# Kernel optimization log

Hardware: AMD Instinct MI355X
Metric: run time of the kernel (lower is better)

Reference implementation:

```python
import jax, jax.numpy as jnp
import numpy as np

N, E = 50000, 800000
D_IN, D_H, D_E, D_P = 128, 64, 64, 64


def _glorot(key, shape):
    lim = (6.0 / (shape[0] + shape[1])) ** 0.5
    return jax.random.uniform(key, shape, jnp.float32, -lim, lim)


def setup_inputs() -> dict:
    key = jax.random.key(0)
    ks = jax.random.split(key, 8)
    x = jax.random.normal(ks[0], (N, D_IN), jnp.float32)
    edge_index = jax.random.randint(ks[1], (2, E), 0, N, dtype=jnp.int64)
    return {
        "x": x,
        "edge_index": edge_index,
        "W1": _glorot(ks[2], (D_IN, D_H)),
        "b1": jnp.zeros((D_H,), jnp.float32),
        "W2": _glorot(ks[3], (D_H, D_E)),
        "b2": jnp.zeros((D_E,), jnp.float32),
        "Wp1": _glorot(ks[4], (D_E, D_E)),
        "bp1": jnp.zeros((D_E,), jnp.float32),
        "Wp2": _glorot(ks[5], (D_E, D_P)),
        "bp2": jnp.zeros((D_P,), jnp.float32),
    }


def gcn_conv(x, src, dst, W, b):
    # PyG GCNConv: h = D^{-1/2}(A+I)D^{-1/2} (x W) + b, self-loops already in src/dst
    n = x.shape[0]
    h = x @ W  # transform first (out_dim < in_dim -> cheaper messages)
    deg = jax.ops.segment_sum(jnp.ones_like(dst, dtype=h.dtype), dst, num_segments=n)
    dinv = jnp.where(deg > 0, jax.lax.rsqrt(deg), 0.0)
    norm = dinv[src] * dinv[dst]  # [E']
    out = jax.ops.segment_sum(h[src] * norm[:, None], dst, num_segments=n)
    return out + b


def reference(x, edge_index, W1, b1, W2, b2, Wp1, bp1, Wp2, bp2):
    n = x.shape[0]
    loops = jnp.arange(n, dtype=edge_index.dtype)
    src = jnp.concatenate([edge_index[0], loops])
    dst = jnp.concatenate([edge_index[1], loops])
    h = jax.nn.relu(gcn_conv(x, src, dst, W1, b1))
    z = gcn_conv(h, src, dst, W2, b2)
    p = jax.nn.relu(z @ Wp1 + bp1) @ Wp2 + bp2
    return (z, p)
```

## Files before the change

### kernel.cpp

```cpp
#include <hip/hip_runtime.h>
#include <hip/hip_fp16.h>

#define DIN 128
#define DH 64
#define NBINS 512
#define BIN_SHIFT 7
#define BIN_NODES 128
#define ETILE 4096
#define EBUF 4096

__device__ inline unsigned pack_half2(float a, float b) {
  __half2 h = __floats2half2_rn(a, b);
  return *(unsigned*)&h;
}
__device__ inline float2 unpack_half2(unsigned u) {
  __half2 h = *(__half2*)&u;
  return __half22float2(h);
}

__global__ __launch_bounds__(512) void k_zero(int* __restrict__ p, int n) {
  int i = blockIdx.x * blockDim.x + threadIdx.x;
  if (i < n) p[i] = 0;
}

__global__ __launch_bounds__(256) void k_fusedA(const float* __restrict__ x,
                                                const float* __restrict__ W1,
                                                __half* __restrict__ g1,
                                                const int* __restrict__ dst,
                                                int* __restrict__ binTot,
                                                int n, int e, int gG) {
  __shared__ float xsT[32][132];
  __shared__ float ws[32 * 64];
  __shared__ int hh[NBINS];
  int t = threadIdx.x;
  int bid = blockIdx.x;

  if (bid >= gG) {
    int b = bid - gG;
    for (int i = t; i < NBINS; i += 256) hh[i] = 0;
    __syncthreads();
    int lo = b * ETILE, hi = lo + ETILE; if (hi > e) hi = e;
    for (int i = lo + t; i < hi; i += 256) atomicAdd(&hh[dst[i] >> BIN_SHIFT], 1);
    __syncthreads();
    for (int i = t; i < NBINS; i += 256) if (hh[i]) atomicAdd(&binTot[i], hh[i]);
    return;
  }

  int row0 = bid * 128;
  int rg = t >> 4, cg = t & 15;
  int r0 = rg * 8, c0 = cg * 4;
  int lr = t >> 3, kq = t & 7;
  float4 acc[8];
#pragma unroll
  for (int i = 0; i < 8; ++i) acc[i] = make_float4(0.f, 0.f, 0.f, 0.f);

  for (int kc = 0; kc < DIN; kc += 32) {
#pragma unroll
    for (int it = 0; it < 4; ++it) {
      int r = it * 32 + lr;
      int gr = row0 + r;
      float4 v = make_float4(0.f, 0.f, 0.f, 0.f);
      if (gr < n) v = *(const float4*)&x[(size_t)gr * DIN + kc + kq * 4];
      xsT[kq * 4 + 0][r] = v.x;
      xsT[kq * 4 + 1][r] = v.y;
      xsT[kq * 4 + 2][r] = v.z;
      xsT[kq * 4 + 3][r] = v.w;
    }
#pragma unroll
    for (int j = 0; j < 8; ++j) ws[t + j * 256] = W1[(size_t)kc * 64 + t + j * 256];
    __syncthreads();
#pragma unroll
    for (int k = 0; k < 32; ++k) {
      float4 xa = *(const float4*)&xsT[k][r0];
      float4 xb = *(const float4*)&xsT[k][r0 + 4];
      float4 wv = *(const float4*)&ws[k * 64 + c0];
      float xr[8] = {xa.x, xa.y, xa.z, xa.w, xb.x, xb.y, xb.z, xb.w};
#pragma unroll
      for (int i = 0; i < 8; ++i) {
        acc[i].x = fmaf(xr[i], wv.x, acc[i].x);
        acc[i].y = fmaf(xr[i], wv.y, acc[i].y);
        acc[i].z = fmaf(xr[i], wv.z, acc[i].z);
        acc[i].w = fmaf(xr[i], wv.w, acc[i].w);
      }
    }
    __syncthreads();
  }
#pragma unroll
  for (int i = 0; i < 8; ++i) {
    int gr = row0 + r0 + i;
    if (gr < n) {
      uint2 u;
      u.x = pack_half2(acc[i].x, acc[i].y);
      u.y = pack_half2(acc[i].z, acc[i].w);
      *(uint2*)&g1[(size_t)gr * 64 + c0] = u;
    }
  }
}

__global__ __launch_bounds__(512) void k_binscan(const int* __restrict__ binTot,
                                                 int* __restrict__ binOff,
                                                 int* __restrict__ binCur, int e) {
  __shared__ int sm[NBINS];
  int t = threadIdx.x;
  int v = binTot[t];
  sm[t] = v;
  __syncthreads();
  for (int ofs = 1; ofs < NBINS; ofs <<= 1) {
    int u = (t >= ofs) ? sm[t - ofs] : 0;
    __syncthreads();
    sm[t] += u;
    __syncthreads();
  }
  int ex = sm[t] - v;
  binOff[t] = ex;
  binCur[t] = ex;
  if (t == NBINS - 1) binOff[NBINS] = sm[NBINS - 1];
}

__global__ __launch_bounds__(256) void k_scatter2(const int* __restrict__ src,
                                                  const int* __restrict__ dst,
                                                  int* __restrict__ binCur,
                                                  int* __restrict__ sp, int e) {
  __shared__ int hh[NBINS];
  __shared__ int base[NBINS];
  int t = threadIdx.x;
  for (int i = t; i < NBINS; i += 256) hh[i] = 0;
  __syncthreads();
  int lo = blockIdx.x * ETILE, hi = lo + ETILE; if (hi > e) hi = e;
  for (int i = lo + t; i < hi; i += 256) atomicAdd(&hh[dst[i] >> BIN_SHIFT], 1);
  __syncthreads();
  for (int i = t; i < NBINS; i += 256) {
    int c = hh[i];
    base[i] = c ? atomicAdd(&binCur[i], c) : 0;
  }
  __syncthreads();
  for (int i = t; i < NBINS; i += 256) hh[i] = 0;
  __syncthreads();
  for (int i = lo + t; i < hi; i += 256) {
    int d = dst[i];
    int bn = d >> BIN_SHIFT;
    int pos = base[bn] + atomicAdd(&hh[bn], 1);
    sp[pos] = (src[i] << BIN_SHIFT) | (d & (BIN_NODES - 1));
  }
}

__global__ __launch_bounds__(256) void k_bincsr(const int* __restrict__ sp,
                                                const int* __restrict__ binOff,
                                                int* __restrict__ off,
                                                float* __restrict__ dinv,
                                                int* __restrict__ srcs,
                                                int n, int e) {
  __shared__ int dl[BIN_NODES];
  __shared__ int sc[BIN_NODES];
  __shared__ int curl[BIN_NODES];
  __shared__ int ebuf[EBUF];
  int b = blockIdx.x, t = threadIdx.x;
  if (t < BIN_NODES) dl[t] = 0;
  __syncthreads();
  int e0 = binOff[b];
  int e1 = binOff[b + 1];
  for (int i = e0 + t; i < e1; i += 256) {
    int u = sp[i];
    int k = i - e0;
    if (k < EBUF) ebuf[k] = u;
    atomicAdd(&dl[u & (BIN_NODES - 1)], 1);
  }
  __syncthreads();
  if (t < BIN_NODES) sc[t] = dl[t];
  __syncthreads();
  for (int ofs = 1; ofs < BIN_NODES; ofs <<= 1) {
    int v = (t < BIN_NODES && t >= ofs) ? sc[t - ofs] : 0;
    __syncthreads();
    if (t < BIN_NODES) sc[t] += v;
    __syncthreads();
  }
  int nbase = b * BIN_NODES;
  if (t < BIN_NODES) {
    int ex = e0 + sc[t] - dl[t];
    curl[t] = ex;
    int node = nbase + t;
    if (node < n) {
      off[node] = ex;
      dinv[node] = rsqrtf((float)(dl[t] + 1));
    }
  }
  if (b == 0 && t == 0) off[n] = e;
  __syncthreads();
  for (int i = e0 + t; i < e1; i += 256) {
    int k = i - e0;
    int u = (k < EBUF) ? ebuf[k] : sp[i];
    int l = u & (BIN_NODES - 1);
    int pos = atomicAdd(&curl[l], 1);
    srcs[pos] = u >> BIN_SHIFT;
  }
}

__global__ __launch_bounds__(256) void k_agg(const __half* __restrict__ gh,
                                             const int* __restrict__ off,
                                             const int* __restrict__ srcs,
                                             const float* __restrict__ dinv,
                                             const float* __restrict__ bias,
                                             __half* __restrict__ out, int n, int relu) {
  int gid = blockIdx.x * 4 + (threadIdx.x >> 6);
  if (gid >= n) return;
  gid = __builtin_amdgcn_readfirstlane(gid);
  int lane = threadIdx.x & 63;
  int grp = lane >> 4;
  int d4 = (lane & 15) * 4;
  float di = dinv[gid];
  float4 acc = make_float4(0.f, 0.f, 0.f, 0.f);
  if (grp == 0) {
    uint2 raw = *(const uint2*)(gh + (size_t)gid * DH + d4);
    float2 f0 = unpack_half2(raw.x), f1 = unpack_half2(raw.y);
    float s = di * di;
    acc.x = f0.x * s; acc.y = f0.y * s; acc.z = f1.x * s; acc.w = f1.y * s;
  }
  int b0 = off[gid], b1 = off[gid + 1];
  int j = b0 + grp;
  for (; j + 12 < b1; j += 16) {
    int s0 = srcs[j], s1 = srcs[j + 4], s2 = srcs[j + 8], s3 = srcs[j + 12];
    float w0 = dinv[s0] * di, w1 = dinv[s1] * di;
    float w2 = dinv[s2] * di, w3 = dinv[s3] * di;
    uint2 r0 = *(const uint2*)(gh + (size_t)s0 * DH + d4);
    uint2 r1 = *(const uint2*)(gh + (size_t)s1 * DH + d4);
    uint2 r2 = *(const uint2*)(gh + (size_t)s2 * DH + d4);
    uint2 r3 = *(const uint2*)(gh + (size_t)s3 * DH + d4);
    float2 a0 = unpack_half2(r0.x), a1 = unpack_half2(r0.y);
    float2 c0 = unpack_half2(r1.x), c1 = unpack_half2(r1.y);
    float2 e0 = unpack_half2(r2.x), e1 = unpack_half2(r2.y);
    float2 g0 = unpack_half2(r3.x), g1 = unpack_half2(r3.y);
    acc.x = fmaf(a0.x, w0, acc.x); acc.y = fmaf(a0.y, w0, acc.y);
    acc.z = fmaf(a1.x, w0, acc.z); acc.w = fmaf(a1.y, w0, acc.w);
    acc.x = fmaf(c0.x, w1, acc.x); acc.y = fmaf(c0.y, w1, acc.y);
    acc.z = fmaf(c1.x, w1, acc.z); acc.w = fmaf(c1.y, w1, acc.w);
    acc.x = fmaf(e0.x, w2, acc.x); acc.y = fmaf(e0.y, w2, acc.y);
    acc.z = fmaf(e1.x, w2, acc.z); acc.w = fmaf(e1.y, w2, acc.w);
    acc.x = fmaf(g0.x, w3, acc.x); acc.y = fmaf(g0.y, w3, acc.y);
    acc.z = fmaf(g1.x, w3, acc.z); acc.w = fmaf(g1.y, w3, acc.w);
  }
  for (; j + 4 < b1; j += 8) {
    int sa = srcs[j], sb = srcs[j + 4];
    float wa = dinv[sa] * di, wb = dinv[sb] * di;
    uint2 ra = *(const uint2*)(gh + (size_t)sa * DH + d4);
    uint2 rb = *(const uint2*)(gh + (size_t)sb * DH + d4);
    float2 a0 = unpack_half2(ra.x), a1 = unpack_half2(ra.y);
    float2 c0 = unpack_half2(rb.x), c1 = unpack_half2(rb.y);
    acc.x = fmaf(a0.x, wa, acc.x); acc.y = fmaf(a0.y, wa, acc.y);
    acc.z = fmaf(a1.x, wa, acc.z); acc.w = fmaf(a1.y, wa, acc.w);
    acc.x = fmaf(c0.x, wb, acc.x); acc.y = fmaf(c0.y, wb, acc.y);
    acc.z = fmaf(c1.x, wb, acc.z); acc.w = fmaf(c1.y, wb, acc.w);
  }
  if (j < b1) {
    int s = srcs[j];
    float w = dinv[s] * di;
    uint2 r = *(const uint2*)(gh + (size_t)s * DH + d4);
    float2 f0 = unpack_half2(r.x), f1 = unpack_half2(r.y);
    acc.x = fmaf(f0.x, w, acc.x); acc.y = fmaf(f0.y, w, acc.y);
    acc.z = fmaf(f1.x, w, acc.z); acc.w = fmaf(f1.y, w, acc.w);
  }
  acc.x += __shfl_xor(acc.x, 16, 64); acc.x += __shfl_xor(acc.x, 32, 64);
  acc.y += __shfl_xor(acc.y, 16, 64); acc.y += __shfl_xor(acc.y, 32, 64);
  acc.z += __shfl_xor(acc.z, 16, 64); acc.z += __shfl_xor(acc.z, 32, 64);
  acc.w += __shfl_xor(acc.w, 16, 64); acc.w += __shfl_xor(acc.w, 32, 64);
  if (lane < 16) {
    if (bias) {
      float4 bv = *(const float4*)&bias[d4];
      acc.x += bv.x; acc.y += bv.y; acc.z += bv.z; acc.w += bv.w;
    }
    if (relu) {
      acc.x = fmaxf(acc.x, 0.f); acc.y = fmaxf(acc.y, 0.f);
      acc.z = fmaxf(acc.z, 0.f); acc.w = fmaxf(acc.w, 0.f);
    }
    uint2 u;
    u.x = pack_half2(acc.x, acc.y);
    u.y = pack_half2(acc.z, acc.w);
    *(uint2*)&out[(size_t)gid * DH + d4] = u;
  }
}

__global__ __launch_bounds__(256) void k_head3(const __half* __restrict__ ah,
                                               const float* __restrict__ W2,
                                               const float* __restrict__ b2,
                                               const float* __restrict__ Wp1,
                                               const float* __restrict__ bp1,
                                               const float* __restrict__ Wp2,
                                               const float* __restrict__ bp2,
                                               float* __restrict__ z,
                                               float* __restrict__ p, int n) {
  constexpr int KC = 32;
  constexpr int MP = 132;
  __shared__ float xsT[KC][MP];
  __shared__ float ws[KC * 64];
  __shared__ float TsT[64][MP];
  int t = threadIdx.x;
  int row0 = blockIdx.x * 128;
  int rg = t >> 4, cg = t & 15;
  int r0 = rg * 8, c0 = cg * 4;
  int lr = t >> 3, kq = t & 7;

  float4 acc[8];
#pragma unroll
  for (int i = 0; i < 8; ++i) acc[i] = make_float4(0.f, 0.f, 0.f, 0.f);
  for (int kc = 0; kc < 64; kc += KC) {
#pragma unroll
    for (int it = 0; it < 4; ++it) {
      int r = it * 32 + lr;
      int gr = row0 + r;
      uint2 v = make_uint2(0u, 0u);
      if (gr < n) v = *(const uint2*)(ah + (size_t)gr * 64 + kc + kq * 4);
      float2 f0 = unpack_half2(v.x), f1 = unpack_half2(v.y);
      xsT[kq * 4 + 0][r] = f0.x;
      xsT[kq * 4 + 1][r] = f0.y;
      xsT[kq * 4 + 2][r] = f1.x;
      xsT[kq * 4 + 3][r] = f1.y;
    }
#pragma unroll
    for (int j = 0; j < 8; ++j) ws[t + j * 256] = W2[(size_t)kc * 64 + t + j * 256];
    __syncthreads();
#pragma unroll
    for (int k = 0; k < KC; ++k) {
      float4 xa = *(const float4*)&xsT[k][r0];
      float4 xb = *(const float4*)&xsT[k][r0 + 4];
      float4 wv = *(const float4*)&ws[k * 64 + c0];
      float xr[8] = {xa.x, xa.y, xa.z, xa.w, xb.x, xb.y, xb.z, xb.w};
#pragma unroll
      for (int i = 0; i < 8; ++i) {
        acc[i].x = fmaf(xr[i], wv.x, acc[i].x);
        acc[i].y = fmaf(xr[i], wv.y, acc[i].y);
        acc[i].z = fmaf(xr[i], wv.z, acc[i].z);
        acc[i].w = fmaf(xr[i], wv.w, acc[i].w);
      }
    }
    __syncthreads();
  }
  {
    float4 bv = *(const float4*)&b2[c0];
#pragma unroll
    for (int i = 0; i < 8; ++i) {
      float4 o = acc[i];
      o.x += bv.x; o.y += bv.y; o.z += bv.z; o.w += bv.w;
      int r = r0 + i;
      int gr = row0 + r;
      if (gr < n) *(float4*)&z[(size_t)gr * 64 + c0] = o;
      TsT[c0 + 0][r] = o.x;
      TsT[c0 + 1][r] = o.y;
      TsT[c0 + 2][r] = o.z;
      TsT[c0 + 3][r] = o.w;
    }
  }

  float4 acc2[8];
#pragma unroll
  for (int i = 0; i < 8; ++i) acc2[i] = make_float4(0.f, 0.f, 0.f, 0.f);
  for (int kc = 0; kc < 64; kc += KC) {
    __syncthreads();
#pragma unroll
    for (int j = 0; j < 8; ++j) ws[t + j * 256] = Wp1[(size_t)kc * 64 + t + j * 256];
    __syncthreads();
#pragma unroll
    for (int k = 0; k < KC; ++k) {
      float4 xa = *(const float4*)&TsT[kc + k][r0];
      float4 xb = *(const float4*)&TsT[kc + k][r0 + 4];
      float4 wv = *(const float4*)&ws[k * 64 + c0];
      float xr[8] = {xa.x, xa.y, xa.z, xa.w, xb.x, xb.y, xb.z, xb.w};
#pragma unroll
      for (int i = 0; i < 8; ++i) {
        acc2[i].x = fmaf(xr[i], wv.x, acc2[i].x);
        acc2[i].y = fmaf(xr[i], wv.y, acc2[i].y);
        acc2[i].z = fmaf(xr[i], wv.z, acc2[i].z);
        acc2[i].w = fmaf(xr[i], wv.w, acc2[i].w);
      }
    }
  }
  __syncthreads();
  {
    float4 bv = *(const float4*)&bp1[c0];
#pragma unroll
    for (int i = 0; i < 8; ++i) {
      int r = r0 + i;
      TsT[c0 + 0][r] = fmaxf(acc2[i].x + bv.x, 0.f);
      TsT[c0 + 1][r] = fmaxf(acc2[i].y + bv.y, 0.f);
      TsT[c0 + 2][r] = fmaxf(acc2[i].z + bv.z, 0.f);
      TsT[c0 + 3][r] = fmaxf(acc2[i].w + bv.w, 0.f);
    }
  }

  float4 acc3[8];
#pragma unroll
  for (int i = 0; i < 8; ++i) acc3[i] = make_float4(0.f, 0.f, 0.f, 0.f);
  for (int kc = 0; kc < 64; kc += KC) {
    __syncthreads();
#pragma unroll
    for (int j = 0; j < 8; ++j) ws[t + j * 256] = Wp2[(size_t)kc * 64 + t + j * 256];
    __syncthreads();
#pragma unroll
    for (int k = 0; k < KC; ++k) {
      float4 xa = *(const float4*)&TsT[kc + k][r0];
      float4 xb = *(const float4*)&TsT[kc + k][r0 + 4];
      float4 wv = *(const float4*)&ws[k * 64 + c0];
      float xr[8] = {xa.x, xa.y, xa.z, xa.w, xb.x, xb.y, xb.z, xb.w};
#pragma unroll
      for (int i = 0; i < 8; ++i) {
        acc3[i].x = fmaf(xr[i], wv.x, acc3[i].x);
        acc3[i].y = fmaf(xr[i], wv.y, acc3[i].y);
        acc3[i].z = fmaf(xr[i], wv.z, acc3[i].z);
        acc3[i].w = fmaf(xr[i], wv.w, acc3[i].w);
      }
    }
  }
  {
    float4 bv = *(const float4*)&bp2[c0];
#pragma unroll
    for (int i = 0; i < 8; ++i) {
      int gr = row0 + r0 + i;
      if (gr < n) {
        float4 o = acc3[i];
        o.x += bv.x; o.y += bv.y; o.z += bv.z; o.w += bv.w;
        *(float4*)&p[(size_t)gr * 64 + c0] = o;
      }
    }
  }
}

extern "C" void kernel_launch(void* const* d_in, const int* in_sizes, int n_in,
                              void* d_out, int out_size, void* d_ws, size_t ws_size,
                              hipStream_t stream) {
  const float* x   = (const float*)d_in[0];
  const int*   ei  = (const int*)d_in[1];
  const float* W1  = (const float*)d_in[2];
  const float* b1  = (const float*)d_in[3];
  const float* W2  = (const float*)d_in[4];
  const float* b2  = (const float*)d_in[5];
  const float* Wp1 = (const float*)d_in[6];
  const float* bp1 = (const float*)d_in[7];
  const float* Wp2 = (const float*)d_in[8];
  const float* bp2 = (const float*)d_in[9];

  int n = in_sizes[0] / DIN;
  int e = in_sizes[1] / 2;
  const int* src = ei;
  const int* dst = ei + e;

  int nblkE = (e + ETILE - 1) / ETILE;
  int nbBins = (n + BIN_NODES - 1) / BIN_NODES;
  int gG = (n + 127) / 128;

  char* ws = (char*)d_ws;
  __half* gtab   = (__half*)ws;
  __half* htab   = (__half*)(ws + ((size_t)7 << 20));
  char*   ctrl   = ws + ((size_t)14 << 20);
  int*    binTot = (int*)(ctrl);
  int*    binOff = (int*)(ctrl + 4096);
  int*    binCur = (int*)(ctrl + 8192);
  int*    off    = (int*)(ctrl + 16384);
  float*  dinv   = (float*)(ctrl + 16384 + (1 << 18));
  int*    sp     = (int*)(ctrl + 16384 + (2 << 18));
  int*    srcs   = sp + e;

  float* zout = (float*)d_out;
  float* pout = zout + (size_t)n * DH;

  k_zero<<<1, 512, 0, stream>>>(binTot, NBINS);

  k_fusedA<<<gG + nblkE, 256, 0, stream>>>(x, W1, gtab, dst, binTot, n, e, gG);

  k_binscan<<<1, 512, 0, stream>>>(binTot, binOff, binCur, e);

  k_scatter2<<<nblkE, 256, 0, stream>>>(src, dst, binCur, sp, e);

  k_bincsr<<<nbBins, 256, 0, stream>>>(sp, binOff, off, dinv, srcs, n, e);

  k_agg<<<(n + 3) / 4, 256, 0, stream>>>(gtab, off, srcs, dinv, b1, htab, n, 1);

  k_agg<<<(n + 3) / 4, 256, 0, stream>>>(htab, off, srcs, dinv, nullptr, gtab, n, 0);

  k_head3<<<gG, 256, 0, stream>>>(gtab, W2, b2, Wp1, bp1, Wp2, bp2, zout, pout, n);
}
```

Baseline: 145.1 us.

## Replace tiled head MLP with per-row wavefront kernel reading weights from global

The three-layer head kernel, which used 128-row tiles with LDS-staged weights and block barriers, is replaced by a 64-thread kernel where each pair of lanes owns one row and half the output columns. Weights are read straight from global memory with float4 loads instead of being staged in shared memory, and no __syncthreads are needed because each wave handles its own rows. This removes barrier and staging overhead and gives many more small blocks. The cost is that every lane reloads the full weight rows through cache, a 32-float accumulator raises register pressure, and the z/p stores are strided per lane and less coalesced.

```diff
diff --git a/kernel.cpp b/kernel.cpp
--- a/kernel.cpp
+++ b/kernel.cpp
@@ -8,6 +8,7 @@
 #define BIN_NODES 128
 #define ETILE 4096
 #define EBUF 4096
+#define HROWS 32
 
 __device__ inline unsigned pack_half2(float a, float b) {
   __half2 h = __floats2half2_rn(a, b);
@@ -278,146 +279,115 @@
   }
 }
 
-__global__ __launch_bounds__(256) void k_head3(const __half* __restrict__ ah,
-                                               const float* __restrict__ W2,
-                                               const float* __restrict__ b2,
-                                               const float* __restrict__ Wp1,
-                                               const float* __restrict__ bp1,
-                                               const float* __restrict__ Wp2,
-                                               const float* __restrict__ bp2,
-                                               float* __restrict__ z,
-                                               float* __restrict__ p, int n) {
-  constexpr int KC = 32;
-  constexpr int MP = 132;
-  __shared__ float xsT[KC][MP];
-  __shared__ float ws[KC * 64];
-  __shared__ float TsT[64][MP];
-  int t = threadIdx.x;
-  int row0 = blockIdx.x * 128;
-  int rg = t >> 4, cg = t & 15;
-  int r0 = rg * 8, c0 = cg * 4;
-  int lr = t >> 3, kq = t & 7;
-
-  float4 acc[8];
-#pragma unroll
-  for (int i = 0; i < 8; ++i) acc[i] = make_float4(0.f, 0.f, 0.f, 0.f);
-  for (int kc = 0; kc < 64; kc += KC) {
-#pragma unroll
-    for (int it = 0; it < 4; ++it) {
-      int r = it * 32 + lr;
-      int gr = row0 + r;
-      uint2 v = make_uint2(0u, 0u);
-      if (gr < n) v = *(const uint2*)(ah + (size_t)gr * 64 + kc + kq * 4);
-      float2 f0 = unpack_half2(v.x), f1 = unpack_half2(v.y);
-      xsT[kq * 4 + 0][r] = f0.x;
-      xsT[kq * 4 + 1][r] = f0.y;
-      xsT[kq * 4 + 2][r] = f1.x;
-      xsT[kq * 4 + 3][r] = f1.y;
-    }
-#pragma unroll
-    for (int j = 0; j < 8; ++j) ws[t + j * 256] = W2[(size_t)kc * 64 + t + j * 256];
-    __syncthreads();
-#pragma unroll
-    for (int k = 0; k < KC; ++k) {
-      float4 xa = *(const float4*)&xsT[k][r0];
-      float4 xb = *(const float4*)&xsT[k][r0 + 4];
-      float4 wv = *(const float4*)&ws[k * 64 + c0];
-      float xr[8] = {xa.x, xa.y, xa.z, xa.w, xb.x, xb.y, xb.z, xb.w};
-#pragma unroll
-      for (int i = 0; i < 8; ++i) {
-        acc[i].x = fmaf(xr[i], wv.x, acc[i].x);
-        acc[i].y = fmaf(xr[i], wv.y, acc[i].y);
-        acc[i].z = fmaf(xr[i], wv.z, acc[i].z);
-        acc[i].w = fmaf(xr[i], wv.w, acc[i].w);
-      }
-    }
-    __syncthreads();
-  }
+__global__ __launch_bounds__(64) void k_head_row(const __half* __restrict__ ah,
+                                                 const float* __restrict__ W2,
+                                                 const float* __restrict__ b2,
+                                                 const float* __restrict__ Wp1,
+                                                 const float* __restrict__ bp1,
+                                                 const float* __restrict__ Wp2,
+                                                 const float* __restrict__ bp2,
+                                                 float* __restrict__ z,
+                                                 float* __restrict__ p, int n) {
+  __shared__ float buf0[HROWS][68];
+  __shared__ float buf1[HROWS][68];
+  int L = threadIdx.x;
+  int m = L >> 1;
+  int h = L & 1;
+  int row = blockIdx.x * HROWS + m;
+  bool valid = row < n;
+  int c0 = h * 32;
+
   {
-    float4 bv = *(const float4*)&b2[c0];
-#pragma unroll
-    for (int i = 0; i < 8; ++i) {
-      float4 o = acc[i];
-      o.x += bv.x; o.y += bv.y; o.z += bv.z; o.w += bv.w;
-      int r = r0 + i;
-      int gr = row0 + r;
-      if (gr < n) *(float4*)&z[(size_t)gr * 64 + c0] = o;
-      TsT[c0 + 0][r] = o.x;
-      TsT[c0 + 1][r] = o.y;
-      TsT[c0 + 2][r] = o.z;
-      TsT[c0 + 3][r] = o.w;
-    }
-  }
-
-  float4 acc2[8];
-#pragma unroll
-  for (int i = 0; i < 8; ++i) acc2[i] = make_float4(0.f, 0.f, 0.f, 0.f);
-  for (int kc = 0; kc < 64; kc += KC) {
-    __syncthreads();
-#pragma unroll
-    for (int j = 0; j < 8; ++j) ws[t + j * 256] = Wp1[(size_t)kc * 64 + t + j * 256];
-    __syncthreads();
-#pragma unroll
-    for (int k = 0; k < KC; ++k) {
-      float4 xa = *(const float4*)&TsT[kc + k][r0];
-      float4 xb = *(const float4*)&TsT[kc + k][r0 + 4];
-      float4 wv = *(const float4*)&ws[k * 64 + c0];
-      float xr[8] = {xa.x, xa.y, xa.z, xa.w, xb.x, xb.y, xb.z, xb.w};
-#pragma unroll
-      for (int i = 0; i < 8; ++i) {
-        acc2[i].x = fmaf(xr[i], wv.x, acc2[i].x);
-        acc2[i].y = fmaf(xr[i], wv.y, acc2[i].y);
-        acc2[i].z = fmaf(xr[i], wv.z, acc2[i].z);
-        acc2[i].w = fmaf(xr[i], wv.w, acc2[i].w);
-      }
-    }
-  }
-  __syncthreads();
+    const __half* ar = ah + (size_t)row * 64 + c0;
+#pragma unroll
+    for (int q = 0; q < 8; ++q) {
+      uint2 u = valid ? *(const uint2*)(ar + q * 4) : make_uint2(0u, 0u);
+      float2 f0 = unpack_half2(u.x), f1 = unpack_half2(u.y);
+      float4* d = (float4*)&buf0[m][c0 + q * 4];
+      *d = make_float4(f0.x, f0.y, f1.x, f1.y);
+    }
+  }
+
+  float acc[32];
+
+#pragma unroll
+  for (int c = 0; c < 32; ++c) acc[c] = 0.f;
+  for (int k = 0; k < 64; ++k) {
+    float a = buf0[m][k];
+    const float4* w = (const float4*)&W2[k * 64 + c0];
+#pragma unroll
+    for (int c4 = 0; c4 < 8; ++c4) {
+      float4 wv = w[c4];
+      acc[c4 * 4 + 0] = fmaf(a, wv.x, acc[c4 * 4 + 0]);
+      acc[c4 * 4 + 1] = fmaf(a, wv.y, acc[c4 * 4 + 1]);
+      acc[c4 * 4 + 2] = fmaf(a, wv.z, acc[c4 * 4 + 2]);
+      acc[c4 * 4 + 3] = fmaf(a, wv.w, acc[c4 * 4 + 3]);
+    }
+  }
   {
-    float4 bv = *(const float4*)&bp1[c0];
-#pragma unroll
-    for (int i = 0; i < 8; ++i) {
-      int r = r0 + i;
-      TsT[c0 + 0][r] = fmaxf(acc2[i].x + bv.x, 0.f);
-      TsT[c0 + 1][r] = fmaxf(acc2[i].y + bv.y, 0.f);
-      TsT[c0 + 2][r] = fmaxf(acc2[i].z + bv.z, 0.f);
-      TsT[c0 + 3][r] = fmaxf(acc2[i].w + bv.w, 0.f);
-    }
-  }
-
-  float4 acc3[8];
-#pragma unroll
-  for (int i = 0; i < 8; ++i) acc3[i] = make_float4(0.f, 0.f, 0.f, 0.f);
-  for (int kc = 0; kc < 64; kc += KC) {
-    __syncthreads();
-#pragma unroll
-    for (int j = 0; j < 8; ++j) ws[t + j * 256] = Wp2[(size_t)kc * 64 + t + j * 256];
-    __syncthreads();
-#pragma unroll
-    for (int k = 0; k < KC; ++k) {
-      float4 xa = *(const float4*)&TsT[kc + k][r0];
-      float4 xb = *(const float4*)&TsT[kc + k][r0 + 4];
-      float4 wv = *(const float4*)&ws[k * 64 + c0];
-      float xr[8] = {xa.x, xa.y, xa.z, xa.w, xb.x, xb.y, xb.z, xb.w};
-#pragma unroll
-      for (int i = 0; i < 8; ++i) {
-        acc3[i].x = fmaf(xr[i], wv.x, acc3[i].x);
-        acc3[i].y = fmaf(xr[i], wv.y, acc3[i].y);
-        acc3[i].z = fmaf(xr[i], wv.z, acc3[i].z);
-        acc3[i].w = fmaf(xr[i], wv.w, acc3[i].w);
-      }
+    const float4* bv = (const float4*)&b2[c0];
+    float* zr = valid ? &z[(size_t)row * 64 + c0] : nullptr;
+#pragma unroll
+    for (int c4 = 0; c4 < 8; ++c4) {
+      float4 b = bv[c4];
+      float4 o = make_float4(acc[c4 * 4 + 0] + b.x, acc[c4 * 4 + 1] + b.y,
+                             acc[c4 * 4 + 2] + b.z, acc[c4 * 4 + 3] + b.w);
+      *(float4*)&buf1[m][c0 + c4 * 4] = o;
+      if (zr) *(float4*)&zr[c4 * 4] = o;
+    }
+  }
+
+#pragma unroll
+  for (int c = 0; c < 32; ++c) acc[c] = 0.f;
+  for (int k = 0; k < 64; ++k) {
+    float a = buf1[m][k];
+    const float4* w = (const float4*)&Wp1[k * 64 + c0];
+#pragma unroll
+    for (int c4 = 0; c4 < 8; ++c4) {
+      float4 wv = w[c4];
+      acc[c4 * 4 + 0] = fmaf(a, wv.x, acc[c4 * 4 + 0]);
+      acc[c4 * 4 + 1] = fmaf(a, wv.y, acc[c4 * 4 + 1]);
+      acc[c4 * 4 + 2] = fmaf(a, wv.z, acc[c4 * 4 + 2]);
+      acc[c4 * 4 + 3] = fmaf(a, wv.w, acc[c4 * 4 + 3]);
     }
   }
   {
-    float4 bv = *(const float4*)&bp2[c0];
-#pragma unroll
-    for (int i = 0; i < 8; ++i) {
-      int gr = row0 + r0 + i;
-      if (gr < n) {
-        float4 o = acc3[i];
-        o.x += bv.x; o.y += bv.y; o.z += bv.z; o.w += bv.w;
-        *(float4*)&p[(size_t)gr * 64 + c0] = o;
-      }
+    const float4* bv = (const float4*)&bp1[c0];
+#pragma unroll
+    for (int c4 = 0; c4 < 8; ++c4) {
+      float4 b = bv[c4];
+      float4 o;
+      o.x = fmaxf(acc[c4 * 4 + 0] + b.x, 0.f);
+      o.y = fmaxf(acc[c4 * 4 + 1] + b.y, 0.f);
+      o.z = fmaxf(acc[c4 * 4 + 2] + b.z, 0.f);
+      o.w = fmaxf(acc[c4 * 4 + 3] + b.w, 0.f);
+      *(float4*)&buf0[m][c0 + c4 * 4] = o;
+    }
+  }
+
+#pragma unroll
+  for (int c = 0; c < 32; ++c) acc[c] = 0.f;
+  for (int k = 0; k < 64; ++k) {
+    float a = buf0[m][k];
+    const float4* w = (const float4*)&Wp2[k * 64 + c0];
+#pragma unroll
+    for (int c4 = 0; c4 < 8; ++c4) {
+      float4 wv = w[c4];
+      acc[c4 * 4 + 0] = fmaf(a, wv.x, acc[c4 * 4 + 0]);
+      acc[c4 * 4 + 1] = fmaf(a, wv.y, acc[c4 * 4 + 1]);
+      acc[c4 * 4 + 2] = fmaf(a, wv.z, acc[c4 * 4 + 2]);
+      acc[c4 * 4 + 3] = fmaf(a, wv.w, acc[c4 * 4 + 3]);
+    }
+  }
+  if (valid) {
+    const float4* bv = (const float4*)&bp2[c0];
+    float* pr = &p[(size_t)row * 64 + c0];
+#pragma unroll
+    for (int c4 = 0; c4 < 8; ++c4) {
+      float4 b = bv[c4];
+      float4 o = make_float4(acc[c4 * 4 + 0] + b.x, acc[c4 * 4 + 1] + b.y,
+                             acc[c4 * 4 + 2] + b.z, acc[c4 * 4 + 3] + b.w);
+      *(float4*)&pr[c4 * 4] = o;
     }
   }
 }
@@ -444,6 +414,7 @@
   int nblkE = (e + ETILE - 1) / ETILE;
   int nbBins = (n + BIN_NODES - 1) / BIN_NODES;
   int gG = (n + 127) / 128;
+  int gH = (n + HROWS - 1) / HROWS;
 
   char* ws = (char*)d_ws;
   __half* gtab   = (__half*)ws;
@@ -474,5 +445,5 @@
 
   k_agg<<<(n + 3) / 4, 256, 0, stream>>>(htab, off, srcs, dinv, nullptr, gtab, n, 0);
 
-  k_head3<<<gG, 256, 0, stream>>>(gtab, W2, b2, Wp1, bp1, Wp2, bp2, zout, pout, n);
-}
+  k_head_row<<<gH, 64, 0, stream>>>(gtab, W2, b2, Wp1, bp1, Wp2, bp2, zout, pout, n);
+}
```

Result: slower. 268.3 us (+84.8%).
